# Performance work log

Hardware: AMD Instinct MI355X
Metric: run time of the kernel (lower is better)

Reference implementation:

```python
import jax, jax.numpy as jnp
import numpy as np

N_LEVELS, CPL = 4, 1024           # levels, cells per level (n_cells = 4096)
IN_D, HID, OUT_D, MLP = 512, 1024, 512, 128


def setup_inputs() -> dict:
    key = jax.random.key(0)
    ks = iter(jax.random.split(key, 32))
    r = lambda shape, s=0.05: jax.random.normal(next(ks), shape, dtype=jnp.float32) * s
    inp = {
        'x': r((1, IN_D), 1.0),
        'hiddens': r((N_LEVELS * CPL, HID), 0.1),
        'ea_W1': r((N_LEVELS, IN_D + HID, MLP)), 'ea_b1': r((N_LEVELS, MLP)),
        'ea_W2': r((N_LEVELS, MLP, OUT_D)),      'ea_b2': r((N_LEVELS, OUT_D)),
        'eg_W1': r((N_LEVELS, IN_D + HID, MLP)), 'eg_b1': r((N_LEVELS, MLP)),
        'eg_W2': r((N_LEVELS, MLP, OUT_D)),      'eg_b2': r((N_LEVELS, OUT_D)),
        'gru_Wih': r((N_LEVELS, 3 * HID, OUT_D + 1)),
        'gru_Whh': r((N_LEVELS, 3 * HID, HID)),
        'gru_bih': r((N_LEVELS, 3 * HID)), 'gru_bhh': r((N_LEVELS, 3 * HID)),
        'pred_W1': r((N_LEVELS - 1, HID, HID)), 'pred_b1': r((N_LEVELS - 1, HID)),
        'pred_W2': r((N_LEVELS - 1, HID, HID)), 'pred_b2': r((N_LEVELS - 1, HID)),
        'pei_W': r((HID * N_LEVELS, OUT_D)), 'pei_b': r((OUT_D,)),
        'step': 10,
    }
    return inp


def _forward(x, hiddens, ea_W1, ea_b1, ea_W2, ea_b2, eg_W1, eg_b1, eg_W2, eg_b2,
             gru_Wih, gru_Whh, gru_bih, gru_bhh, pred_W1, pred_b1, pred_W2, pred_b2,
             pei_W, pei_b, step):
    L = gru_Whh.shape[0]
    Hd = gru_Whh.shape[2]
    C = hiddens.shape[0] // L
    h = hiddens.reshape(L, C, Hd)                              # [L,C,H]
    xb = jnp.broadcast_to(x[0], (L, C, x.shape[-1]))           # same x for every cell
    comb = jnp.concatenate([xb, h], axis=-1)                   # [L,C,IN+H]

    def mlp(W1, b1, W2, b2):
        z = jax.nn.relu(jnp.einsum('lci,lim->lcm', comb, W1) + b1[:, None, :])
        return jnp.einsum('lcm,lmo->lco', z, W2) + b2[:, None, :]

    out = mlp(ea_W1, ea_b1, ea_W2, ea_b2) - mlp(eg_W1, eg_b1, eg_W2, eg_b2)  # a - g
    tension = jnp.mean(out ** 2, axis=-1, keepdims=True)       # [L,C,1]
    avg_tension = jnp.mean(tension)                            # mean over all cells

    # GRUCell (torch gate order r,z,n); mem input is detached in the original
    mem_in = jax.lax.stop_gradient(jnp.concatenate([out, tension], axis=-1))  # [L,C,OUT+1]
    gi = jnp.einsum('lci,lgi->lcg', mem_in, gru_Wih) + gru_bih[:, None, :]
    gh = jnp.einsum('lch,lgh->lcg', h, gru_Whh) + gru_bhh[:, None, :]
    i_r, i_z, i_n = jnp.split(gi, 3, axis=-1)
    h_r, h_z, h_n = jnp.split(gh, 3, axis=-1)
    rg = jax.nn.sigmoid(i_r + h_r)
    zg = jax.nn.sigmoid(i_z + h_z)
    ng = jnp.tanh(i_n + rg * h_n)
    new_h = jax.lax.stop_gradient((1.0 - zg) * ng + zg * h)    # self.hiddens = ...detach()

    level_means = new_h.mean(axis=1)                           # [L,H] (pre pe-update)

    # top-down predictors: predicted[lv] from level_means[lv+1]
    pz = jax.nn.relu(jnp.einsum('li,lim->lm', level_means[1:], pred_W1) + pred_b1)
    predicted = jnp.einsum('lm,lmo->lo', pz, pred_W2) + pred_b2          # [L-1,H]
    pe_signal = jax.lax.stop_gradient((predicted - level_means[:-1]) * 0.05)
    delta = jnp.zeros_like(level_means).at[:-1].add(pe_signal).at[1:].add(-0.5 * pe_signal)
    hh = new_h + delta[:, None, :]

    # per-level mean blend
    hh = 0.85 * hh + 0.15 * hh.mean(axis=1, keepdims=True)
    # faction sync: with n_factions == n_levels, factions == levels exactly
    hh = 0.85 * hh + 0.15 * hh.mean(axis=1, keepdims=True)
    if step > 5:  # debate (step is a static Python int)
        global_op = hh.mean(axis=1).mean(axis=0)               # [H]
        dc = max(1, C // 4)
        hh = hh.at[:, :dc].set(0.85 * hh[:, :dc] + 0.15 * global_op)

    combined = level_means.reshape(-1) @ pei_W + pei_b         # [OUT]
    return combined, avg_tension, hh.reshape(-1, Hd)


def reference(x, hiddens, ea_W1, ea_b1, ea_W2, ea_b2, eg_W1, eg_b1, eg_W2, eg_b2,
              gru_Wih, gru_Whh, gru_bih, gru_bhh, pred_W1, pred_b1, pred_W2, pred_b2,
              pei_W, pei_b, step):
    return _forward(x, hiddens, ea_W1, ea_b1, ea_W2, ea_b2, eg_W1, eg_b1, eg_W2, eg_b2,
                    gru_Wih, gru_Whh, gru_bih, gru_bhh, pred_W1, pred_b1, pred_W2, pred_b2,
                    pei_W, pei_b, step)
```

## Files before the change

kernel.cpp:

```cpp
#include <hip/hip_runtime.h>
#include <math.h>

#define L4   4
#define CPL  1024
#define HID  1024
#define IND  512
#define MLPD 128
#define OUTD 512
#define G3   3072
#define ROWS 4096
#define KP   544
#define SCL  0.0009765625f

typedef unsigned short u16;
typedef u16   u16x8  __attribute__((ext_vector_type(8)));
typedef short bf16x8 __attribute__((ext_vector_type(8)));
typedef float f32x4  __attribute__((ext_vector_type(4)));

__device__ __forceinline__ float b2f(u16 u) {
  return __uint_as_float(((unsigned int)u) << 16);
}
__device__ __forceinline__ u16 f2b(float f) {
  unsigned int x = __float_as_uint(f);
  x += 0x7fffu + ((x >> 16) & 1u);
  return (u16)(x >> 16);
}
__device__ __forceinline__ float sigm(float v) { return 1.0f/(1.0f + expf(-v)); }

__device__ __forceinline__ float ld1(const void* p, size_t i, bool f32) {
  return f32 ? ((const float*)p)[i] : b2f(((const u16*)p)[i]);
}
__device__ __forceinline__ void st1(void* p, size_t i, float v, bool f32) {
  if (f32) ((float*)p)[i] = v; else ((u16*)p)[i] = f2b(v);
}
__device__ __forceinline__ u16x8 ldc8(const void* p, size_t i, bool f32) {
  u16x8 r;
  if (f32) {
    const float* q = (const float*)p + i;
    float4 v0 = *reinterpret_cast<const float4*>(q);
    float4 v1 = *reinterpret_cast<const float4*>(q + 4);
    r[0]=f2b(v0.x); r[1]=f2b(v0.y); r[2]=f2b(v0.z); r[3]=f2b(v0.w);
    r[4]=f2b(v1.x); r[5]=f2b(v1.y); r[6]=f2b(v1.z); r[7]=f2b(v1.w);
  } else {
    r = *reinterpret_cast<const u16x8*>((const u16*)p + i);
  }
  return r;
}

__global__ void k_detect(const void* __restrict__ x, int* __restrict__ flag) {
  int t = threadIdx.x;
  const u16* xu = (const u16*)x;
  unsigned u = xu[2*t];
  int e = (u >> 7) & 0xFF;
  int good = (e >= 96 && e <= 134) ? 1 : 0;
  __shared__ int cnt[256];
  cnt[t] = good;
  __syncthreads();
  for (int s = 128; s > 0; s >>= 1) { if (t < s) cnt[t] += cnt[t+s]; __syncthreads(); }
  if (t == 0) flag[0] = (cnt[0] < 200) ? 1 : 0;
}

__global__ void k_prep(float* __restrict__ zf, const void* __restrict__ bih,
                       const void* __restrict__ bhh, const int* __restrict__ dflag,
                       float* __restrict__ bs_r, float* __restrict__ bs_z,
                       float* __restrict__ bn_i, float* __restrict__ bn_h) {
  const bool f32 = dflag[0] != 0;
  int b = blockIdx.x, t = threadIdx.x;
  if (b < 16) {
    int idx = b*256 + t;
    int l = idx >> 10, j = idx & 1023;
    bs_r[idx] = ld1(bih, l*G3 + j, f32)        + ld1(bhh, l*G3 + j, f32);
    bs_z[idx] = ld1(bih, l*G3 + 1024 + j, f32) + ld1(bhh, l*G3 + 1024 + j, f32);
    bn_i[idx] = ld1(bih, l*G3 + 2048 + j, f32);
    bn_h[idx] = ld1(bhh, l*G3 + 2048 + j, f32);
  } else {
    int idx = (b-16)*256 + t;
    zf[idx] = 0.0f;
  }
}

__global__ void k_prep_wih(const void* __restrict__ Wih, const int* __restrict__ dflag,
                           u16* __restrict__ WihP) {
  const bool f32 = dflag[0] != 0;
  int row = blockIdx.x;
  int t = threadIdx.x;
  size_t src = (size_t)row * 513;
  size_t dst = (size_t)row * KP;
  WihP[dst + t]       = f2b(ld1(Wih, src + t, f32));
  WihP[dst + 256 + t] = f2b(ld1(Wih, src + 256 + t, f32));
  if (t < 32) {
    float v = (t == 0) ? ld1(Wih, src + 512, f32) : 0.0f;
    WihP[dst + 512 + t] = f2b(v);
  }
}

__global__ void k_prep_cvt(const void* __restrict__ Whh, const void* __restrict__ H,
                           const int* __restrict__ dflag,
                           u16* __restrict__ WhhP, u16* __restrict__ HB) {
  const bool f32 = dflag[0] != 0;
  int t = threadIdx.x;
  int b = blockIdx.x;
  int c8 = (t & 127) * 8;
  if (b < 6144) {
    int row = b*2 + (t >> 7);
    size_t off = (size_t)row * HID + c8;
    *reinterpret_cast<u16x8*>(&WhhP[off]) = ldc8(Whh, off, f32);
  } else {
    int row = (b - 6144)*2 + (t >> 7);
    size_t off = (size_t)row * HID + c8;
    *reinterpret_cast<u16x8*>(&HB[off]) = ldc8(H, off, f32);
  }
}

__global__ void k_prep_w1t(const void* __restrict__ eaW1, const void* __restrict__ egW1,
                           const int* __restrict__ dflag, u16* __restrict__ W1T) {
  const bool f32 = dflag[0] != 0;
  __shared__ u16 sT[128*66];
  int l = blockIdx.x, path = blockIdx.y, kt = blockIdx.z;
  int t = threadIdx.x;
  const void* W1 = path ? egW1 : eaW1;
  for (int rr = 0; rr < 64; rr += 2) {
    int r = rr + (t >> 7), m = t & 127;
    float v = ld1(W1, ((size_t)l*1536 + 512 + kt*64 + r)*MLPD + m, f32);
    sT[m*66 + r] = f2b(v);
  }
  __syncthreads();
  for (int mm = 0; mm < 128; mm += 4) {
    int m = mm + (t >> 6), kk = t & 63;
    W1T[((size_t)l*256 + path*128 + m)*1024 + kt*64 + kk] = sT[m*66 + kk];
  }
}

__global__ void k_prep_w2m(const void* __restrict__ eaW2, const void* __restrict__ egW2,
                           const int* __restrict__ dflag, u16* __restrict__ W2M) {
  const bool f32 = dflag[0] != 0;
  __shared__ u16 sT[128*130];
  int l = blockIdx.x, path = blockIdx.y, ot = blockIdx.z;
  int t = threadIdx.x;
  const void* W2 = path ? egW2 : eaW2;
  float sgn = path ? -1.0f : 1.0f;
  for (int rr = 0; rr < 128; rr += 2) {
    int r = rr + (t >> 7), o = t & 127;
    float v = ld1(W2, ((size_t)l*MLPD + r)*OUTD + ot*128 + o, f32);
    sT[o*130 + r] = f2b(sgn*v);
  }
  __syncthreads();
  for (int oo = 0; oo < 128; oo += 2) {
    int o = oo + (t >> 7), m = t & 127;
    W2M[((size_t)l*OUTD + ot*128 + o)*256 + path*128 + m] = sT[o*130 + m];
  }
}

__global__ void k_base_acc(const void* __restrict__ x, const void* __restrict__ eaW1,
                           const void* __restrict__ egW1, const int* __restrict__ dflag,
                           float* __restrict__ baseacc) {
  const bool f32 = dflag[0] != 0;
  int l = blockIdx.x, path = blockIdx.y, kc = blockIdx.z, m = threadIdx.x;
  const void* W1 = path ? egW1 : eaW1;
  float acc = 0.0f;
  int i0 = kc*128;
  for (int i = i0; i < i0 + 128; ++i)
    acc += ld1(x, i, f32) * ld1(W1, ((size_t)l*1536 + i)*MLPD + m, f32);
  atomicAdd(&baseacc[path*512 + l*MLPD + m], acc);
}

#define SWZ(row, ku) ((row)*64 + ((ku) ^ (((row)&7)<<3)))

__global__ __launch_bounds__(256) void k_z_mfma(
    const u16* __restrict__ HB, const u16* __restrict__ W1T,
    const void* __restrict__ eab1, const void* __restrict__ egb1,
    const float* __restrict__ baseacc, const int* __restrict__ dflag,
    u16* __restrict__ Z) {
  const bool f32 = dflag[0] != 0;
  __shared__ __align__(16) u16 sA[2][64*64];
  __shared__ __align__(16) u16 sB[2][64*64];
  int t = threadIdx.x;
  int row0 = blockIdx.x * 64;
  int n0   = blockIdx.y * 64;
  int l    = row0 >> 10;
  int wid = t >> 6, lane = t & 63;
  int waveM = wid >> 1, waveN = wid & 1;
  int quad = lane >> 4, lcol = lane & 15;

  f32x4 acc[2][2];
  const f32x4 zz = {0.0f,0.0f,0.0f,0.0f};
#pragma unroll
  for (int i = 0; i < 2; ++i)
#pragma unroll
    for (int j = 0; j < 2; ++j) acc[i][j] = zz;

  u16x8 ra[2], rb[2];
  auto loadk = [&](int k0) {
#pragma unroll
    for (int s = 0; s < 2; ++s) {
      int idx = s*256 + t, row = idx >> 3, ch = idx & 7;
      ra[s] = *reinterpret_cast<const u16x8*>(
          HB + (size_t)(row0 + row)*HID + k0 + ch*8);
      rb[s] = *reinterpret_cast<const u16x8*>(
          W1T + ((size_t)l*256 + n0 + row)*1024 + k0 + ch*8);
    }
  };
  auto stage = [&](int cb) {
#pragma unroll
    for (int s = 0; s < 2; ++s) {
      int idx = s*256 + t, row = idx >> 3, ch = idx & 7;
      *reinterpret_cast<u16x8*>(&sA[cb][SWZ(row, ch*8)]) = ra[s];
      *reinterpret_cast<u16x8*>(&sB[cb][SWZ(row, ch*8)]) = rb[s];
    }
  };

  int cur = 0;
  loadk(0);
  for (int k0 = 0; k0 < HID; k0 += 64) {
    stage(cur);
    asm volatile("s_waitcnt lgkmcnt(0)" ::: "memory");
    __builtin_amdgcn_s_barrier();
    if (k0 + 64 < HID) loadk(k0 + 64);
    __builtin_amdgcn_s_setprio(1);
#pragma unroll
    for (int kc = 0; kc < 2; ++kc) {
      bf16x8 af[2];
#pragma unroll
      for (int i = 0; i < 2; ++i) {
        int rl = waveM*32 + i*16 + lcol;
        af[i] = *reinterpret_cast<const bf16x8*>(&sA[cur][SWZ(rl, kc*32 + quad*8)]);
      }
#pragma unroll
      for (int j = 0; j < 2; ++j) {
        int jl = waveN*32 + j*16 + lcol;
        bf16x8 bf = *reinterpret_cast<const bf16x8*>(&sB[cur][SWZ(jl, kc*32 + quad*8)]);
#pragma unroll
        for (int i = 0; i < 2; ++i)
          acc[i][j] = __builtin_amdgcn_mfma_f32_16x16x32_bf16(af[i], bf, acc[i][j], 0, 0, 0);
      }
    }
    __builtin_amdgcn_s_setprio(0);
    cur ^= 1;
  }
#pragma unroll
  for (int j = 0; j < 2; ++j) {
    int nn = n0 + waveN*32 + j*16 + lcol;
    int path = nn >> 7, m = nn & 127;
    float bval = baseacc[path*512 + l*MLPD + m] +
                 ld1(path ? egb1 : eab1, l*MLPD + m, f32);
#pragma unroll
    for (int i = 0; i < 2; ++i)
#pragma unroll
      for (int g = 0; g < 4; ++g) {
        int r = row0 + waveM*32 + i*16 + quad*4 + g;
        float v = acc[i][j][g] + bval;
        Z[(size_t)r*256 + nn] = f2b(v > 0.0f ? v : 0.0f);
      }
  }
}

__global__ __launch_bounds__(256) void k_outm(
    const u16* __restrict__ Zb, const u16* __restrict__ W2M,
    const void* __restrict__ eab2, const void* __restrict__ egb2,
    const int* __restrict__ dflag, u16* __restrict__ OUTT) {
  const bool f32 = dflag[0] != 0;
  __shared__ __align__(16) u16 sA[2][128*64];
  __shared__ __align__(16) u16 sB[2][64*64];
  int t = threadIdx.x;
  int row0 = blockIdx.x * 128;
  int n0   = blockIdx.y * 64;
  int l    = row0 >> 10;
  int wid = t >> 6, lane = t & 63;
  int waveM = wid & 1, waveJ = wid >> 1;
  int quad = lane >> 4, lcol = lane & 15;

  f32x4 acc[4][2];
  const f32x4 zz = {0.0f,0.0f,0.0f,0.0f};
#pragma unroll
  for (int i = 0; i < 4; ++i)
#pragma unroll
    for (int j = 0; j < 2; ++j) acc[i][j] = zz;

  u16x8 ra[4], rb[2];
  auto loadk = [&](int k0) {
#pragma unroll
    for (int s = 0; s < 4; ++s) {
      int idx = s*256 + t, row = idx >> 3, ch = idx & 7;
      ra[s] = *reinterpret_cast<const u16x8*>(
          Zb + (size_t)(row0 + row)*256 + k0 + ch*8);
    }
#pragma unroll
    for (int s = 0; s < 2; ++s) {
      int idx = s*256 + t, row = idx >> 3, ch = idx & 7;
      rb[s] = *reinterpret_cast<const u16x8*>(
          W2M + ((size_t)l*OUTD + n0 + row)*256 + k0 + ch*8);
    }
  };
  auto stage = [&](int cb) {
#pragma unroll
    for (int s = 0; s < 4; ++s) {
      int idx = s*256 + t, row = idx >> 3, ch = idx & 7;
      *reinterpret_cast<u16x8*>(&sA[cb][SWZ(row, ch*8)]) = ra[s];
    }
#pragma unroll
    for (int s = 0; s < 2; ++s) {
      int idx = s*256 + t, row = idx >> 3, ch = idx & 7;
      *reinterpret_cast<u16x8*>(&sB[cb][SWZ(row, ch*8)]) = rb[s];
    }
  };

  int cur = 0;
  loadk(0);
  for (int k0 = 0; k0 < 256; k0 += 64) {
    stage(cur);
    asm volatile("s_waitcnt lgkmcnt(0)" ::: "memory");
    __builtin_amdgcn_s_barrier();
    if (k0 + 64 < 256) loadk(k0 + 64);
    __builtin_amdgcn_s_setprio(1);
#pragma unroll
    for (int kc = 0; kc < 2; ++kc) {
      bf16x8 af[4];
#pragma unroll
      for (int i = 0; i < 4; ++i) {
        int rl = waveM*64 + i*16 + lcol;
        af[i] = *reinterpret_cast<const bf16x8*>(&sA[cur][SWZ(rl, kc*32 + quad*8)]);
      }
#pragma unroll
      for (int jj = 0; jj < 2; ++jj) {
        int jl = waveJ*32 + jj*16 + lcol;
        bf16x8 bf = *reinterpret_cast<const bf16x8*>(&sB[cur][SWZ(jl, kc*32 + quad*8)]);
#pragma unroll
        for (int i = 0; i < 4; ++i)
          acc[i][jj] = __builtin_amdgcn_mfma_f32_16x16x32_bf16(af[i], bf, acc[i][jj], 0, 0, 0);
      }
    }
    __builtin_amdgcn_s_setprio(0);
    cur ^= 1;
  }
#pragma unroll
  for (int jj = 0; jj < 2; ++jj) {
    int o = n0 + waveJ*32 + jj*16 + lcol;
    float bd = ld1(eab2, l*OUTD + o, f32) - ld1(egb2, l*OUTD + o, f32);
#pragma unroll
    for (int i = 0; i < 4; ++i)
#pragma unroll
      for (int g = 0; g < 4; ++g) {
        int r = row0 + waveM*64 + i*16 + quad*4 + g;
        OUTT[(size_t)r*KP + o] = f2b(acc[i][jj][g] + bd);
      }
  }
}

__global__ void k_tension(u16* __restrict__ OUTT, float* __restrict__ tsum) {
  int row = blockIdx.x, t = threadIdx.x;
  u16* p = OUTT + (size_t)row*KP;
  float v0 = b2f(p[t]), v1 = b2f(p[t+256]);
  float s = v0*v0 + v1*v1;
#pragma unroll
  for (int off = 32; off > 0; off >>= 1) s += __shfl_down(s, off, 64);
  __shared__ float red[4];
  if ((t & 63) == 0) red[t >> 6] = s;
  __syncthreads();
  if (t == 0) {
    float tot = red[0] + red[1] + red[2] + red[3];
    p[512] = f2b(tot * (1.0f/512.0f));
    atomicAdd(tsum, tot);
  }
  if (t < 31) p[513 + t] = 0;
}

#define GRULOAD(P, s) do {                                                     \
    if ((s) < 9) {                                                             \
      int k0 = (s)*64, kw = KP - k0;                                           \
      bool ok = ch8 < kw;                                                      \
      const u16* pA = OUTT + (size_t)row0*KP + k0 + ch8;                       \
      P##a0 = ok ? *(const u16x8*)(pA + (size_t)(arow     )*KP) : z8;          \
      P##a1 = ok ? *(const u16x8*)(pA + (size_t)(arow + 32)*KP) : z8;          \
      P##a2 = ok ? *(const u16x8*)(pA + (size_t)(arow + 64)*KP) : z8;          \
      P##a3 = ok ? *(const u16x8*)(pA + (size_t)(arow + 96)*KP) : z8;          \
      const u16* pB = WihP + ((size_t)l*G3 + j0)*KP + k0 + ch8;                \
      P##b0 = ok ? *(const u16x8*)(pB + (size_t)(   0 + arow     )*KP) : z8;   \
      P##b1 = ok ? *(const u16x8*)(pB + (size_t)(   0 + arow + 32)*KP) : z8;   \
      P##b2 = ok ? *(const u16x8*)(pB + (size_t)(1024 + arow     )*KP) : z8;   \
      P##b3 = ok ? *(const u16x8*)(pB + (size_t)(1024 + arow + 32)*KP) : z8;   \
      P##b4 = ok ? *(const u16x8*)(pB + (size_t)(2048 + arow     )*KP) : z8;   \
      P##b5 = ok ? *(const u16x8*)(pB + (size_t)(2048 + arow + 32)*KP) : z8;   \
    } else {                                                                   \
      int k0 = ((s) - 9)*64;                                                   \
      const u16* pA = HB + (size_t)row0*HID + k0 + ch8;                        \
      P##a0 = *(const u16x8*)(pA + (size_t)(arow     )*HID);                   \
      P##a1 = *(const u16x8*)(pA + (size_t)(arow + 32)*HID);                   \
      P##a2 = *(const u16x8*)(pA + (size_t)(arow + 64)*HID);                   \
      P##a3 = *(const u16x8*)(pA + (size_t)(arow + 96)*HID);                   \
      const u16* pB = WhhP + ((size_t)l*G3 + j0)*HID + k0 + ch8;               \
      P##b0 = *(const u16x8*)(pB + (size_t)(   0 + arow     )*HID);            \
      P##b1 = *(const u16x8*)(pB + (size_t)(   0 + arow + 32)*HID);            \
      P##b2 = *(const u16x8*)(pB + (size_t)(1024 + arow     )*HID);            \
      P##b3 = *(const u16x8*)(pB + (size_t)(1024 + arow + 32)*HID);            \
      P##b4 = *(const u16x8*)(pB + (size_t)(2048 + arow     )*HID);            \
      P##b5 = *(const u16x8*)(pB + (size_t)(2048 + arow + 32)*HID);            \
    }                                                                          \
  } while (0)

#define GRUSTAGE(P, cb) do {                                                   \
    *(u16x8*)&sA[cb][SWZ(arow,      ch8)] = P##a0;                             \
    *(u16x8*)&sA[cb][SWZ(arow + 32, ch8)] = P##a1;                             \
    *(u16x8*)&sA[cb][SWZ(arow + 64, ch8)] = P##a2;                             \
    *(u16x8*)&sA[cb][SWZ(arow + 96, ch8)] = P##a3;                             \
    *(u16x8*)&sB[cb][0*4096 + SWZ(arow,      ch8)] = P##b0;                    \
    *(u16x8*)&sB[cb][0*4096 + SWZ(arow + 32, ch8)] = P##b1;                    \
    *(u16x8*)&sB[cb][1*4096 + SWZ(arow,      ch8)] = P##b2;                    \
    *(u16x8*)&sB[cb][1*4096 + SWZ(arow + 32, ch8)] = P##b3;                    \
    *(u16x8*)&sB[cb][2*4096 + SWZ(arow,      ch8)] = P##b4;                    \
    *(u16x8*)&sB[cb][2*4096 + SWZ(arow + 32, ch8)] = P##b5;                    \
  } while (0)

__global__ __launch_bounds__(256, 2) void k_gru_mfma(
    const u16* __restrict__ OUTT, const u16* __restrict__ HB,
    const u16* __restrict__ WihP, const u16* __restrict__ WhhP,
    const void* __restrict__ H,
    const float* __restrict__ bs_r, const float* __restrict__ bs_z,
    const float* __restrict__ bn_i, const float* __restrict__ bn_h,
    const int* __restrict__ dflag, void* __restrict__ outv) {
  const bool f32 = dflag[0] != 0;
  __shared__ __align__(16) u16 sA[2][128*64];
  __shared__ __align__(16) u16 sB[2][3*64*64];
  int t = threadIdx.x;
  int bid = blockIdx.x;
  int xg = bid & 7, inner = bid >> 3;
  int l = xg & 3, jG = xg >> 2;
  int rbi = inner & 7, jbl = inner >> 3;
  int row0 = (l*8 + rbi) * 128;
  int j0   = (jG*8 + jbl) * 64;
  int wid = t >> 6, lane = t & 63;
  int waveM = wid & 1, waveJ = wid >> 1;
  int quad = lane >> 4, lcol = lane & 15;
  int arow = t >> 3, ch8 = (t & 7)*8;

  f32x4 acc[4][4][2];
  const f32x4 zz = {0.0f,0.0f,0.0f,0.0f};
#pragma unroll
  for (int b = 0; b < 4; ++b)
#pragma unroll
    for (int i = 0; i < 4; ++i)
#pragma unroll
      for (int j = 0; j < 2; ++j) acc[b][i][j] = zz;

  const u16x8 z8 = {0,0,0,0,0,0,0,0};
  u16x8 SA_a0, SA_a1, SA_a2, SA_a3, SA_b0, SA_b1, SA_b2, SA_b3, SA_b4, SA_b5;
  u16x8 SB_a0, SB_a1, SB_a2, SB_a3, SB_b0, SB_b1, SB_b2, SB_b3, SB_b4, SB_b5;

  auto domfma = [&](int cb, bool g2) {
    __builtin_amdgcn_s_setprio(1);
#pragma unroll
    for (int kc = 0; kc < 2; ++kc) {
      bf16x8 af[4];
#pragma unroll
      for (int i = 0; i < 4; ++i) {
        int rl = waveM*64 + i*16 + lcol;
        af[i] = *reinterpret_cast<const bf16x8*>(&sA[cb][SWZ(rl, kc*32 + quad*8)]);
      }
#pragma unroll
      for (int b = 0; b < 3; ++b) {
        int ai = (g2 && b == 2) ? 3 : b;
#pragma unroll
        for (int jj = 0; jj < 2; ++jj) {
          int jl = waveJ*32 + jj*16 + lcol;
          bf16x8 bf = *reinterpret_cast<const bf16x8*>(
              &sB[cb][b*4096 + SWZ(jl, kc*32 + quad*8)]);
#pragma unroll
          for (int i = 0; i < 4; ++i)
            acc[ai][i][jj] = __builtin_amdgcn_mfma_f32_16x16x32_bf16(
                af[i], bf, acc[ai][i][jj], 0, 0, 0);
        }
      }
    }
    __builtin_amdgcn_s_setprio(0);
  };

  const int NS = 25;
  int cur = 0;
  GRULOAD(SA_, 0);
  GRULOAD(SB_, 1);
  for (int s = 0; s < NS; s += 2) {
    GRUSTAGE(SA_, cur);
    asm volatile("s_waitcnt lgkmcnt(0)" ::: "memory");
    __builtin_amdgcn_s_barrier();
    if (s + 2 < NS) GRULOAD(SA_, s + 2);
    domfma(cur, s >= 9);
    cur ^= 1;
    if (s + 1 < NS) {
      GRUSTAGE(SB_, cur);
      asm volatile("s_waitcnt lgkmcnt(0)" ::: "memory");
      __builtin_amdgcn_s_barrier();
      if (s + 3 < NS) GRULOAD(SB_, s + 3);
      domfma(cur, s + 1 >= 9);
      cur ^= 1;
    }
  }
#pragma unroll
  for (int i = 0; i < 4; ++i)
#pragma unroll
    for (int jj = 0; jj < 2; ++jj) {
      int j = j0 + waveJ*32 + jj*16 + lcol;
      float br = bs_r[l*HID + j], bz = bs_z[l*HID + j];
      float bi = bn_i[l*HID + j], bh = bn_h[l*HID + j];
#pragma unroll
      for (int g = 0; g < 4; ++g) {
        int r = row0 + waveM*64 + i*16 + quad*4 + g;
        float rg = sigm(acc[0][i][jj][g] + br);
        float zg = sigm(acc[1][i][jj][g] + bz);
        float ng = tanhf(acc[2][i][jj][g] + bi + rg*(acc[3][i][jj][g] + bh));
        float hv = ld1(H, (size_t)r*HID + j, f32);
        st1(outv, 513 + (size_t)r*HID + j, (1.0f - zg)*ng + zg*hv, f32);
      }
    }
}

__global__ void k_lm_acc(const void* __restrict__ outv, const int* __restrict__ dflag,
                         float* __restrict__ lm) {
  const bool f32 = dflag[0] != 0;
  int l = blockIdx.x, cc = blockIdx.y, t = threadIdx.x;
  float s0=0.f, s1=0.f, s2=0.f, s3=0.f;
  for (int c = cc*16; c < cc*16 + 16; ++c) {
    size_t base = 513 + (size_t)(l*CPL + c)*HID;
    s0 += ld1(outv, base + t,       f32);
    s1 += ld1(outv, base + 256 + t, f32);
    s2 += ld1(outv, base + 512 + t, f32);
    s3 += ld1(outv, base + 768 + t, f32);
  }
  atomicAdd(&lm[l*HID + t],       s0);
  atomicAdd(&lm[l*HID + 256 + t], s1);
  atomicAdd(&lm[l*HID + 512 + t], s2);
  atomicAdd(&lm[l*HID + 768 + t], s3);
}

__global__ void k_pz_acc(const float* __restrict__ lm, const void* __restrict__ pW1,
                         const int* __restrict__ dflag, float* __restrict__ pz) {
  const bool f32 = dflag[0] != 0;
  int lv = blockIdx.x, mb = blockIdx.y, kc = blockIdx.z;
  int m = mb*256 + threadIdx.x;
  float acc = 0.0f;
  int i0 = kc*32;
  const float* lmp = lm + (lv + 1)*HID;
  for (int i = i0; i < i0 + 32; ++i)
    acc += lmp[i] * ld1(pW1, ((size_t)lv*HID + i)*HID + m, f32);
  atomicAdd(&pz[lv*HID + m], acc * SCL);
}
__global__ void k_pe_acc(const float* __restrict__ pz, const void* __restrict__ pb1,
                         const void* __restrict__ pW2,
                         const int* __restrict__ dflag, float* __restrict__ pe) {
  const bool f32 = dflag[0] != 0;
  int lv = blockIdx.x, ob = blockIdx.y, kc = blockIdx.z;
  int o = ob*256 + threadIdx.x;
  float acc = 0.0f;
  int m0 = kc*32;
  for (int m = m0; m < m0 + 32; ++m) {
    float v = pz[lv*HID + m] + ld1(pb1, lv*HID + m, f32);
    v = v > 0.0f ? v : 0.0f;
    acc += v * ld1(pW2, ((size_t)lv*HID + m)*HID + o, f32);
  }
  atomicAdd(&pe[lv*HID + o], acc);
}

__global__ void k_addc_gop(const float* __restrict__ lm, const float* __restrict__ pe,
                           const void* __restrict__ pb2, const int* __restrict__ dflag,
                           float* __restrict__ addc, float* __restrict__ gop) {
  const bool f32 = dflag[0] != 0;
  int j = blockIdx.x*256 + threadIdx.x;
  float pe0 = (pe[j]        + ld1(pb2, j,        f32) - lm[j]*SCL)        * 0.05f;
  float pe1 = (pe[1024 + j] + ld1(pb2, 1024 + j, f32) - lm[1024 + j]*SCL) * 0.05f;
  float pe2 = (pe[2048 + j] + ld1(pb2, 2048 + j, f32) - lm[2048 + j]*SCL) * 0.05f;
  float d0 = pe0, d1 = pe1 - 0.5f*pe0, d2 = pe2 - 0.5f*pe1, d3 = -0.5f*pe2;
  float l0 = lm[j]*SCL, l1 = lm[1024 + j]*SCL, l2 = lm[2048 + j]*SCL, l3 = lm[3072 + j]*SCL;
  addc[j]        = 0.2775f*l0 + d0;
  addc[1024 + j] = 0.2775f*l1 + d1;
  addc[2048 + j] = 0.2775f*l2 + d2;
  addc[3072 + j] = 0.2775f*l3 + d3;
  gop[j] = 0.25f*((l0 + d0) + (l1 + d1) + (l2 + d2) + (l3 + d3));
}

__global__ void k_comb_acc(const float* __restrict__ lm, const void* __restrict__ peiW,
                           const int* __restrict__ dflag, float* __restrict__ comb) {
  const bool f32 = dflag[0] != 0;
  int ob = blockIdx.x, kc = blockIdx.y;
  int o = ob*256 + threadIdx.x;
  float acc = 0.0f;
  int i0 = kc*128;
  for (int i = i0; i < i0 + 128; ++i)
    acc += lm[i] * ld1(peiW, (size_t)i*OUTD + o, f32);
  atomicAdd(&comb[o], acc * SCL);
}
__global__ void k_fin(const float* __restrict__ comb, const void* __restrict__ peib,
                      const float* __restrict__ tsum, const int* __restrict__ dflag,
                      void* __restrict__ outv) {
  const bool f32 = dflag[0] != 0;
  int o = blockIdx.x*256 + threadIdx.x;
  st1(outv, o, comb[o] + ld1(peib, o, f32), f32);
  if (o == 0) st1(outv, 512, tsum[0] * (1.0f/(4096.0f*512.0f)), f32);
}

__global__ void k_hh(void* __restrict__ outv, const float* __restrict__ addc,
                     const float* __restrict__ gop, const int* __restrict__ step,
                     const int* __restrict__ dflag) {
  const bool f32 = dflag[0] != 0;
  int row = blockIdx.x, t = threadIdx.x;
  int l = row >> 10, c = row & 1023;
  bool debate = (step[0] > 5) && (c < 256);
  size_t base = 513 + (size_t)row*HID;
#pragma unroll
  for (int k = 0; k < 4; ++k) {
    int j = t + k*256;
    float v = 0.7225f * ld1(outv, base + j, f32) + addc[l*HID + j];
    if (debate) v = 0.85f*v + 0.15f*gop[j];
    st1(outv, base + j, v, f32);
  }
}

extern "C" void kernel_launch(void* const* d_in, const int* in_sizes, int n_in,
                              void* d_out, int out_size, void* d_ws, size_t ws_size,
                              hipStream_t stream) {
  (void)in_sizes; (void)n_in; (void)out_size; (void)ws_size;
  const void* x    = d_in[0];
  const void* hid  = d_in[1];
  const void* eaW1 = d_in[2];
  const void* eab1 = d_in[3];
  const void* eaW2 = d_in[4];
  const void* eab2 = d_in[5];
  const void* egW1 = d_in[6];
  const void* egb1 = d_in[7];
  const void* egW2 = d_in[8];
  const void* egb2 = d_in[9];
  const void* gWih = d_in[10];
  const void* gWhh = d_in[11];
  const void* gbih = d_in[12];
  const void* gbhh = d_in[13];
  const void* pW1  = d_in[14];
  const void* pb1  = d_in[15];
  const void* pW2  = d_in[16];
  const void* pb2  = d_in[17];
  const void* peiW = d_in[18];
  const void* peib = d_in[19];
  const int*  step = (const int*)d_in[20];

  float* wsf = (float*)d_ws;
  float* tsum    = wsf + 0;
  float* baseacc = wsf + 64;
  float* lm      = wsf + 1088;
  float* pz      = wsf + 5184;
  float* pe      = wsf + 8256;
  float* comb    = wsf + 11328;
  int*   dflag   = (int*)(wsf + 12288);
  float* bs_r    = wsf + 12352;
  float* bs_z    = wsf + 16448;
  float* bn_i    = wsf + 20544;
  float* bn_h    = wsf + 24640;
  float* addc    = wsf + 28736;
  float* gop     = wsf + 32832;
  u16* Zb   = (u16*)(wsf + 33856);
  u16* OUTT = Zb + (size_t)4096*256;
  u16* WihP = OUTT + (size_t)4096*KP;
  u16* HB   = WihP + (size_t)12288*KP;
  u16* WhhP = HB   + (size_t)4096*1024;
  u16* W2M  = WhhP + (size_t)12288*1024;
  u16* W1T  = OUTT;

  k_detect   <<<dim3(1),        dim3(256), 0, stream>>>(x, dflag);
  k_prep     <<<dim3(64),       dim3(256), 0, stream>>>(wsf, gbih, gbhh, dflag,
                                                        bs_r, bs_z, bn_i, bn_h);
  k_prep_wih <<<dim3(12288),    dim3(256), 0, stream>>>(gWih, dflag, WihP);
  k_prep_cvt <<<dim3(8192),     dim3(256), 0, stream>>>(gWhh, hid, dflag, WhhP, HB);
  k_prep_w1t <<<dim3(4,2,16),   dim3(256), 0, stream>>>(eaW1, egW1, dflag, W1T);
  k_prep_w2m <<<dim3(4,2,4),    dim3(256), 0, stream>>>(eaW2, egW2, dflag, W2M);
  k_base_acc <<<dim3(4,2,4),    dim3(128), 0, stream>>>(x, eaW1, egW1, dflag, baseacc);
  k_z_mfma   <<<dim3(64,4),     dim3(256), 0, stream>>>(HB, W1T, eab1, egb1,
                                                        baseacc, dflag, Zb);
  k_outm     <<<dim3(32,8),     dim3(256), 0, stream>>>(Zb, W2M, eab2, egb2,
                                                        dflag, OUTT);
  k_tension  <<<dim3(4096),     dim3(256), 0, stream>>>(OUTT, tsum);
  k_gru_mfma <<<dim3(512),      dim3(256), 0, stream>>>(OUTT, HB, WihP, WhhP, hid,
                                                        bs_r, bs_z, bn_i, bn_h,
                                                        dflag, d_out);
  k_lm_acc   <<<dim3(4,64),     dim3(256), 0, stream>>>(d_out, dflag, lm);
  k_pz_acc   <<<dim3(3,4,32),   dim3(256), 0, stream>>>(lm, pW1, dflag, pz);
  k_pe_acc   <<<dim3(3,4,32),   dim3(256), 0, stream>>>(pz, pb1, pW2, dflag, pe);
  k_addc_gop <<<dim3(4),        dim3(256), 0, stream>>>(lm, pe, pb2, dflag, addc, gop);
  k_comb_acc <<<dim3(2,32),     dim3(256), 0, stream>>>(lm, peiW, dflag, comb);
  k_fin      <<<dim3(2),        dim3(256), 0, stream>>>(comb, peib, tsum, dflag, d_out);
  k_hh       <<<dim3(4096),     dim3(256), 0, stream>>>(d_out, addc, gop, step, dflag);
}
```

Measured before the change: 469.1 us.

## Stream GRU GEMM tiles directly to LDS with global_load_lds double buffering

Replaces the register-staged global→register→LDS copy in the GRU MFMA kernel with direct global_load_lds DMA into a unified double-buffered shared array, with pre-swizzled source addresses so the LDS layout matches the existing SWZ pattern. The pipeline moves from a two-stage register prefetch to one barrier per K-step with the next tile issued after the barrier. It also skips the second k-chunk on the partial last Wih step instead of zero-filling. This frees the VGPRs used for staging and removes ds_write instructions, but waits on vmcnt(0) each step, which may expose more load latency.

Result: no change. 467.7 us (-0.3%).

```diff
diff --git a/kernel.cpp b/kernel.cpp
--- a/kernel.cpp
+++ b/kernel.cpp
@@ -16,6 +16,9 @@
 typedef u16   u16x8  __attribute__((ext_vector_type(8)));
 typedef short bf16x8 __attribute__((ext_vector_type(8)));
 typedef float f32x4  __attribute__((ext_vector_type(4)));
+
+typedef __attribute__((address_space(3))) unsigned int lu32;
+typedef const __attribute__((address_space(1))) unsigned int gu32;
 
 __device__ __forceinline__ float b2f(u16 u) {
   return __uint_as_float(((unsigned int)u) << 16);
@@ -364,50 +367,19 @@
   if (t < 31) p[513 + t] = 0;
 }
 
-#define GRULOAD(P, s) do {                                                     \
-    if ((s) < 9) {                                                             \
-      int k0 = (s)*64, kw = KP - k0;                                           \
-      bool ok = ch8 < kw;                                                      \
-      const u16* pA = OUTT + (size_t)row0*KP + k0 + ch8;                       \
-      P##a0 = ok ? *(const u16x8*)(pA + (size_t)(arow     )*KP) : z8;          \
-      P##a1 = ok ? *(const u16x8*)(pA + (size_t)(arow + 32)*KP) : z8;          \
-      P##a2 = ok ? *(const u16x8*)(pA + (size_t)(arow + 64)*KP) : z8;          \
-      P##a3 = ok ? *(const u16x8*)(pA + (size_t)(arow + 96)*KP) : z8;          \
-      const u16* pB = WihP + ((size_t)l*G3 + j0)*KP + k0 + ch8;                \
-      P##b0 = ok ? *(const u16x8*)(pB + (size_t)(   0 + arow     )*KP) : z8;   \
-      P##b1 = ok ? *(const u16x8*)(pB + (size_t)(   0 + arow + 32)*KP) : z8;   \
-      P##b2 = ok ? *(const u16x8*)(pB + (size_t)(1024 + arow     )*KP) : z8;   \
-      P##b3 = ok ? *(const u16x8*)(pB + (size_t)(1024 + arow + 32)*KP) : z8;   \
-      P##b4 = ok ? *(const u16x8*)(pB + (size_t)(2048 + arow     )*KP) : z8;   \
-      P##b5 = ok ? *(const u16x8*)(pB + (size_t)(2048 + arow + 32)*KP) : z8;   \
-    } else {                                                                   \
-      int k0 = ((s) - 9)*64;                                                   \
-      const u16* pA = HB + (size_t)row0*HID + k0 + ch8;                        \
-      P##a0 = *(const u16x8*)(pA + (size_t)(arow     )*HID);                   \
-      P##a1 = *(const u16x8*)(pA + (size_t)(arow + 32)*HID);                   \
-      P##a2 = *(const u16x8*)(pA + (size_t)(arow + 64)*HID);                   \
-      P##a3 = *(const u16x8*)(pA + (size_t)(arow + 96)*HID);                   \
-      const u16* pB = WhhP + ((size_t)l*G3 + j0)*HID + k0 + ch8;               \
-      P##b0 = *(const u16x8*)(pB + (size_t)(   0 + arow     )*HID);            \
-      P##b1 = *(const u16x8*)(pB + (size_t)(   0 + arow + 32)*HID);            \
-      P##b2 = *(const u16x8*)(pB + (size_t)(1024 + arow     )*HID);            \
-      P##b3 = *(const u16x8*)(pB + (size_t)(1024 + arow + 32)*HID);            \
-      P##b4 = *(const u16x8*)(pB + (size_t)(2048 + arow     )*HID);            \
-      P##b5 = *(const u16x8*)(pB + (size_t)(2048 + arow + 32)*HID);            \
+#define GRUISSUE(s, cb) do {                                                   \
+    _Pragma("unroll")                                                          \
+    for (int q = 0; q < 10; ++q) {                                             \
+      lu32* ldst = (lu32*)&sS[cb][(wid*10 + q)*512];                           \
+      if ((s) < 9) {                                                           \
+        if ((s) != 8 || kuq[q] < 32)                                           \
+          __builtin_amdgcn_global_load_lds((gu32*)(q1[q] + (s)*64),            \
+                                           ldst, 16, 0, 0);                    \
+      } else {                                                                 \
+        __builtin_amdgcn_global_load_lds((gu32*)(q2[q] + ((s)-9)*64),          \
+                                         ldst, 16, 0, 0);                      \
+      }                                                                        \
     }                                                                          \
-  } while (0)
-
-#define GRUSTAGE(P, cb) do {                                                   \
-    *(u16x8*)&sA[cb][SWZ(arow,      ch8)] = P##a0;                             \
-    *(u16x8*)&sA[cb][SWZ(arow + 32, ch8)] = P##a1;                             \
-    *(u16x8*)&sA[cb][SWZ(arow + 64, ch8)] = P##a2;                             \
-    *(u16x8*)&sA[cb][SWZ(arow + 96, ch8)] = P##a3;                             \
-    *(u16x8*)&sB[cb][0*4096 + SWZ(arow,      ch8)] = P##b0;                    \
-    *(u16x8*)&sB[cb][0*4096 + SWZ(arow + 32, ch8)] = P##b1;                    \
-    *(u16x8*)&sB[cb][1*4096 + SWZ(arow,      ch8)] = P##b2;                    \
-    *(u16x8*)&sB[cb][1*4096 + SWZ(arow + 32, ch8)] = P##b3;                    \
-    *(u16x8*)&sB[cb][2*4096 + SWZ(arow,      ch8)] = P##b4;                    \
-    *(u16x8*)&sB[cb][2*4096 + SWZ(arow + 32, ch8)] = P##b5;                    \
   } while (0)
 
 __global__ __launch_bounds__(256, 2) void k_gru_mfma(
@@ -418,8 +390,7 @@
     const float* __restrict__ bn_i, const float* __restrict__ bn_h,
     const int* __restrict__ dflag, void* __restrict__ outv) {
   const bool f32 = dflag[0] != 0;
-  __shared__ __align__(16) u16 sA[2][128*64];
-  __shared__ __align__(16) u16 sB[2][3*64*64];
+  __shared__ __align__(16) u16 sS[2][20480];
   int t = threadIdx.x;
   int bid = blockIdx.x;
   int xg = bid & 7, inner = bid >> 3;
@@ -430,7 +401,6 @@
   int wid = t >> 6, lane = t & 63;
   int waveM = wid & 1, waveJ = wid >> 1;
   int quad = lane >> 4, lcol = lane & 15;
-  int arow = t >> 3, ch8 = (t & 7)*8;
 
   f32x4 acc[4][4][2];
   const f32x4 zz = {0.0f,0.0f,0.0f,0.0f};
@@ -441,57 +411,66 @@
 #pragma unroll
       for (int j = 0; j < 2; ++j) acc[b][i][j] = zz;
 
-  const u16x8 z8 = {0,0,0,0,0,0,0,0};
-  u16x8 SA_a0, SA_a1, SA_a2, SA_a3, SA_b0, SA_b1, SA_b2, SA_b3, SA_b4, SA_b5;
-  u16x8 SB_a0, SB_a1, SB_a2, SB_a3, SB_b0, SB_b1, SB_b2, SB_b3, SB_b4, SB_b5;
-
-  auto domfma = [&](int cb, bool g2) {
-    __builtin_amdgcn_s_setprio(1);
-#pragma unroll
-    for (int kc = 0; kc < 2; ++kc) {
-      bf16x8 af[4];
-#pragma unroll
-      for (int i = 0; i < 4; ++i) {
-        int rl = waveM*64 + i*16 + lcol;
-        af[i] = *reinterpret_cast<const bf16x8*>(&sA[cb][SWZ(rl, kc*32 + quad*8)]);
-      }
-#pragma unroll
-      for (int b = 0; b < 3; ++b) {
-        int ai = (g2 && b == 2) ? 3 : b;
-#pragma unroll
-        for (int jj = 0; jj < 2; ++jj) {
-          int jl = waveJ*32 + jj*16 + lcol;
-          bf16x8 bf = *reinterpret_cast<const bf16x8*>(
-              &sB[cb][b*4096 + SWZ(jl, kc*32 + quad*8)]);
-#pragma unroll
-          for (int i = 0; i < 4; ++i)
-            acc[ai][i][jj] = __builtin_amdgcn_mfma_f32_16x16x32_bf16(
-                af[i], bf, acc[ai][i][jj], 0, 0, 0);
-        }
-      }
-    }
-    __builtin_amdgcn_s_setprio(0);
+  const u16* q1[10];
+  const u16* q2[10];
+  int kuq[10];
+#pragma unroll
+  for (int q = 0; q < 10; ++q) {
+    int c = wid*10 + q;
+    int cu = c*512 + lane*8;
+    if (cu < 8192) {
+      int row = cu >> 6, ks = cu & 63;
+      int ku = ks ^ ((row & 7) << 3);
+      kuq[q] = ku;
+      q1[q] = OUTT + (size_t)(row0 + row)*KP + ku;
+      q2[q] = HB   + (size_t)(row0 + row)*HID + ku;
+    } else {
+      int ub = cu - 8192;
+      int rowf = ub >> 6, ks = ub & 63;
+      int band = rowf >> 6, brow = rowf & 63;
+      int ku = ks ^ ((brow & 7) << 3);
+      kuq[q] = ku;
+      size_t gr = (size_t)l*G3 + band*1024 + j0 + brow;
+      q1[q] = WihP + gr*KP + ku;
+      q2[q] = WhhP + gr*HID + ku;
+    }
+  }
+
+  auto domfma_kc = [&](int cb, bool g2, int kc) {
+    bf16x8 af[4];
+#pragma unroll
+    for (int i = 0; i < 4; ++i) {
+      int rl = waveM*64 + i*16 + lcol;
+      af[i] = *reinterpret_cast<const bf16x8*>(&sS[cb][SWZ(rl, kc*32 + quad*8)]);
+    }
+#pragma unroll
+    for (int b = 0; b < 3; ++b) {
+      int ai = (g2 && b == 2) ? 3 : b;
+#pragma unroll
+      for (int jj = 0; jj < 2; ++jj) {
+        int jl = waveJ*32 + jj*16 + lcol;
+        bf16x8 bf = *reinterpret_cast<const bf16x8*>(
+            &sS[cb][8192 + b*4096 + SWZ(jl, kc*32 + quad*8)]);
+#pragma unroll
+        for (int i = 0; i < 4; ++i)
+          acc[ai][i][jj] = __builtin_amdgcn_mfma_f32_16x16x32_bf16(
+              af[i], bf, acc[ai][i][jj], 0, 0, 0);
+      }
+    }
   };
 
   const int NS = 25;
   int cur = 0;
-  GRULOAD(SA_, 0);
-  GRULOAD(SB_, 1);
-  for (int s = 0; s < NS; s += 2) {
-    GRUSTAGE(SA_, cur);
-    asm volatile("s_waitcnt lgkmcnt(0)" ::: "memory");
+  GRUISSUE(0, 0);
+  for (int s = 0; s < NS; ++s) {
+    asm volatile("s_waitcnt vmcnt(0)" ::: "memory");
     __builtin_amdgcn_s_barrier();
-    if (s + 2 < NS) GRULOAD(SA_, s + 2);
-    domfma(cur, s >= 9);
+    if (s + 1 < NS) GRUISSUE(s + 1, cur ^ 1);
+    __builtin_amdgcn_s_setprio(1);
+    domfma_kc(cur, s >= 9, 0);
+    if (s != 8) domfma_kc(cur, s >= 9, 1);
+    __builtin_amdgcn_s_setprio(0);
     cur ^= 1;
-    if (s + 1 < NS) {
-      GRUSTAGE(SB_, cur);
-      asm volatile("s_waitcnt lgkmcnt(0)" ::: "memory");
-      __builtin_amdgcn_s_barrier();
-      if (s + 3 < NS) GRULOAD(SB_, s + 3);
-      domfma(cur, s + 1 >= 9);
-      cur ^= 1;
-    }
   }
 #pragma unroll
   for (int i = 0; i < 4; ++i)
```
